# Performance work log

Hardware: AMD Instinct MI355X
Metric: run time of the kernel (lower is better)

Reference implementation:

```python
import jax, jax.numpy as jnp
import numpy as np

EPS = 1e-8

def _squash(t, axis=-1):
    sq = jnp.sum(t * t, axis=axis, keepdims=True)
    return (sq / (1.0 + sq)) * t / jnp.sqrt(sq + EPS)

def setup_inputs() -> dict:
    key = jax.random.key(0)
    k1, k2 = jax.random.split(key)
    B, IC, NC, OD, ID = 128, 2048, 16, 16, 8
    x = jax.random.normal(k1, (B, IC, ID), dtype=jnp.float32)
    W = 0.01 * jax.random.normal(k2, (1, IC, NC, OD, ID), dtype=jnp.float32)
    return {"x": x, "W": W}

def reference(x, W):
    # u_hat[b,i,c,o] = sum_d W[0,i,c,o,d] * x[b,i,d]
    u_hat = jnp.einsum('icod,bid->bico', W[0], x)  # [B, IC, NC, OD]
    B, IC, NC, _ = u_hat.shape
    b_ij = jnp.zeros((B, IC, NC, 1), dtype=u_hat.dtype)
    v_j = None
    for _ in range(3):  # fixed 3 routing iterations
        c_ij = jax.nn.softmax(b_ij, axis=2)                 # [B, IC, NC, 1]
        s_j = jnp.sum(c_ij * u_hat, axis=1, keepdims=True)  # [B, 1, NC, OD]
        v_j = _squash(s_j, axis=-1)                          # [B, 1, NC, OD]
        b_ij = b_ij + jnp.sum(u_hat * v_j, axis=-1, keepdims=True)
    return jnp.squeeze(v_j, axis=1)  # [B, NC, OD]
```

## Files before the change

### kernel.cpp

```cpp
#include <hip/hip_runtime.h>
#include <math.h>

#define IC_   2048
#define NC_   16
#define OD_   16
#define ID_   8
#define B_    128
#define LOG2E_ 1.4426950408889634f

#define P1_BB   8
#define P1_CH   64
#define P1_ICPB (IC_/P1_CH)
#define P2_NCH  16

typedef _Float16 h2 __attribute__((ext_vector_type(2)));
typedef _Float16 h8 __attribute__((ext_vector_type(8)));

__device__ __forceinline__ int origco(int lane, int k) {
  return ((lane & 15) << 4) + (lane >> 4) + 4 * k;
}

template<int CTRL>
__device__ __forceinline__ float dpp_add(float x) {
  const int xi = __builtin_bit_cast(int, x);
  const int yi = __builtin_amdgcn_update_dpp(xi, xi, CTRL, 0xF, 0xF, false);
  return x + __builtin_bit_cast(float, yi);
}
__device__ __forceinline__ float row16_sum(float x) {
  x = dpp_add<0x0B1>(x);
  x = dpp_add<0x04E>(x);
  x = dpp_add<0x141>(x);
  x = dpp_add<0x140>(x);
  return x;
}

__device__ __forceinline__ float dot8h(h8 w, h8 x) {
  const h2 w0 = __builtin_shufflevector(w, w, 0, 1), x0 = __builtin_shufflevector(x, x, 0, 1);
  const h2 w1 = __builtin_shufflevector(w, w, 2, 3), x1 = __builtin_shufflevector(x, x, 2, 3);
  const h2 w2 = __builtin_shufflevector(w, w, 4, 5), x2 = __builtin_shufflevector(x, x, 4, 5);
  const h2 w3 = __builtin_shufflevector(w, w, 6, 7), x3 = __builtin_shufflevector(x, x, 6, 7);
  float s = __builtin_amdgcn_fdot2(w0, x0, 0.f, false);
  s = __builtin_amdgcn_fdot2(w1, x1, s, false);
  s = __builtin_amdgcn_fdot2(w2, x2, s, false);
  s = __builtin_amdgcn_fdot2(w3, x3, s, false);
  return s;
}

__device__ __forceinline__ unsigned int packh2(float a, float b) {
  h2 h; h[0] = (_Float16)a; h[1] = (_Float16)b;
  return __builtin_bit_cast(unsigned int, h);
}

__global__ __launch_bounds__(256)
void cvtWX(const float* __restrict__ W, const float* __restrict__ x,
           _Float16* __restrict__ Wh, _Float16* __restrict__ xh) {
  if (blockIdx.x < 2048) {
    const int idx = blockIdx.x * 256 + threadIdx.x;
    const int ro  = idx & 255;
    const int i   = idx >> 8;
    const int rp  = (ro >> 4) + ((ro & 3) << 4) + (((ro >> 2) & 3) << 6);
    const float4 a = ((const float4*)W)[2 * idx];
    const float4 b = ((const float4*)W)[2 * idx + 1];
    h8 h;
    h[0] = (_Float16)a.x; h[1] = (_Float16)a.y; h[2] = (_Float16)a.z; h[3] = (_Float16)a.w;
    h[4] = (_Float16)b.x; h[5] = (_Float16)b.y; h[6] = (_Float16)b.z; h[7] = (_Float16)b.w;
    *(h8*)(Wh + ((size_t)i * 256 + rp) * ID_) = h;
  } else {
    const int idx = (blockIdx.x - 2048) * 256 + threadIdx.x;
    const float4 a = ((const float4*)x)[2 * idx];
    const float4 b = ((const float4*)x)[2 * idx + 1];
    h8 h;
    h[0] = (_Float16)a.x; h[1] = (_Float16)a.y; h[2] = (_Float16)a.z; h[3] = (_Float16)a.w;
    h[4] = (_Float16)b.x; h[5] = (_Float16)b.y; h[6] = (_Float16)b.z; h[7] = (_Float16)b.w;
    ((h8*)xh)[idx] = h;
  }
}

__global__ __launch_bounds__(256)
void caps_pass1(const _Float16* __restrict__ xh, const _Float16* __restrict__ Wp,
                unsigned int* __restrict__ u_hat, float* __restrict__ s_part) {
  const int bg = blockIdx.x;
  const int ch = blockIdx.y;
  const int tid = threadIdx.x, wid = tid >> 6, lane = tid & 63;

  float acc[P1_BB][4];
#pragma unroll
  for (int bb = 0; bb < P1_BB; ++bb)
#pragma unroll
    for (int k = 0; k < 4; ++k) acc[bb][k] = 0.f;

  for (int t = 0; t < 4; ++t) {
    const int ip = ch * P1_ICPB + t * 8 + wid * 2;
    const _Float16* wr0 = Wp + (size_t)ip * 2048 + lane * ID_;
    const _Float16* wr1 = wr0 + 2048;
    const h8 wA0 = *(const h8*)(wr0);
    const h8 wA1 = *(const h8*)(wr0 + 512);
    const h8 wA2 = *(const h8*)(wr0 + 1024);
    const h8 wA3 = *(const h8*)(wr0 + 1536);
    const h8 wB0 = *(const h8*)(wr1);
    const h8 wB1 = *(const h8*)(wr1 + 512);
    const h8 wB2 = *(const h8*)(wr1 + 1024);
    const h8 wB3 = *(const h8*)(wr1 + 1536);

#pragma unroll
    for (int bb = 0; bb < P1_BB; ++bb) {
      const int b = bg * P1_BB + bb;
      const _Float16* xp = xh + ((size_t)b * IC_ + ip) * ID_;
      const h8 xv0 = *(const h8*)(xp);
      const h8 xv1 = *(const h8*)(xp + ID_);

      const float u00 = dot8h(wA0, xv0);
      const float u01 = dot8h(wA1, xv0);
      const float u02 = dot8h(wA2, xv0);
      const float u03 = dot8h(wA3, xv0);
      const float u10 = dot8h(wB0, xv1);
      const float u11 = dot8h(wB1, xv1);
      const float u12 = dot8h(wB2, xv1);
      const float u13 = dot8h(wB3, xv1);

      acc[bb][0] += u00 + u10;
      acc[bb][1] += u01 + u11;
      acc[bb][2] += u02 + u12;
      acc[bb][3] += u03 + u13;

      uint4 q;
      q.x = packh2(u00, u01);
      q.y = packh2(u02, u03);
      q.z = packh2(u10, u11);
      q.w = packh2(u12, u13);
      *(uint4*)(u_hat + ((size_t)b * 1024 + (ip >> 1)) * 256 + lane * 4) = q;
    }
  }

  __shared__ float red[4][P1_BB][272];
#pragma unroll
  for (int bb = 0; bb < P1_BB; ++bb)
#pragma unroll
    for (int k = 0; k < 4; ++k)
      red[wid][bb][((lane >> 4) + 4 * k) * 17 + (lane & 15)] = acc[bb][k];
  __syncthreads();
#pragma unroll
  for (int bb = 0; bb < P1_BB; ++bb) {
    const int addr = (tid & 15) * 17 + (tid >> 4);
    const float s = red[0][bb][addr] + red[1][bb][addr] + red[2][bb][addr] + red[3][bb][addr];
    s_part[((size_t)(bg * P1_BB + bb) * P1_CH + ch) * 256 + tid] = s;
  }
}

__global__ __launch_bounds__(256)
void caps_wpass(const unsigned int* __restrict__ u_hat, const float* __restrict__ vs,
                float* __restrict__ s_part) {
  const int b   = blockIdx.x;
  const int ich = blockIdx.y;
  const int tid = threadIdx.x, wid = tid >> 6, lane = tid & 63;

  const float vv0 = vs[b * 256 + origco(lane, 0)];
  const float vv1 = vs[b * 256 + origco(lane, 1)];
  const float vv2 = vs[b * 256 + origco(lane, 2)];
  const float vv3 = vs[b * 256 + origco(lane, 3)];

  float a0 = 0.f, a1 = 0.f, a2 = 0.f, a3 = 0.f;
  const unsigned int* up =
      u_hat + ((size_t)b * 1024 + ich * 64 + wid * 16) * 256 + lane * 4;

#pragma unroll 4
  for (int t = 0; t < 16; ++t) {
    const uint4 q = *(const uint4*)(up + (size_t)t * 256);

    {
      const h2 ha = __builtin_bit_cast(h2, q.x);
      const h2 hb = __builtin_bit_cast(h2, q.y);
      const float u0 = (float)ha[0], u1 = (float)ha[1];
      const float u2 = (float)hb[0], u3 = (float)hb[1];
      float p = u0 * vv0;
      p = fmaf(u1, vv1, p);
      p = fmaf(u2, vv2, p);
      p = fmaf(u3, vv3, p);
      p += __shfl_xor(p, 16);
      p += __shfl_xor(p, 32);
      const float e = __builtin_amdgcn_exp2f(p);
      const float Z = row16_sum(e);
      const float w = e * __builtin_amdgcn_rcpf(Z);
      a0 = fmaf(w, u0, a0);
      a1 = fmaf(w, u1, a1);
      a2 = fmaf(w, u2, a2);
      a3 = fmaf(w, u3, a3);
    }
    {
      const h2 ha = __builtin_bit_cast(h2, q.z);
      const h2 hb = __builtin_bit_cast(h2, q.w);
      const float u0 = (float)ha[0], u1 = (float)ha[1];
      const float u2 = (float)hb[0], u3 = (float)hb[1];
      float p = u0 * vv0;
      p = fmaf(u1, vv1, p);
      p = fmaf(u2, vv2, p);
      p = fmaf(u3, vv3, p);
      p += __shfl_xor(p, 16);
      p += __shfl_xor(p, 32);
      const float e = __builtin_amdgcn_exp2f(p);
      const float Z = row16_sum(e);
      const float w = e * __builtin_amdgcn_rcpf(Z);
      a0 = fmaf(w, u0, a0);
      a1 = fmaf(w, u1, a1);
      a2 = fmaf(w, u2, a2);
      a3 = fmaf(w, u3, a3);
    }
  }

  __shared__ float red[4][272];
  red[wid][((lane >> 4) + 0) * 17 + (lane & 15)]  = a0;
  red[wid][((lane >> 4) + 4) * 17 + (lane & 15)]  = a1;
  red[wid][((lane >> 4) + 8) * 17 + (lane & 15)]  = a2;
  red[wid][((lane >> 4) + 12) * 17 + (lane & 15)] = a3;
  __syncthreads();
  const int addr = (tid & 15) * 17 + (tid >> 4);
  const float s = red[0][addr] + red[1][addr] + red[2][addr] + red[3][addr];
  s_part[((size_t)b * P2_NCH + ich) * 256 + tid] = s;
}

__global__ __launch_bounds__(256)
void caps_reduce(const float* __restrict__ s_part, float* __restrict__ vraw,
                 float* __restrict__ vs_next, float* __restrict__ out,
                 const float* __restrict__ v_prev_raw, float scale, int mode, int nch) {
  const int b = blockIdx.x, t = threadIdx.x;
  float s = 0.f;
  for (int ch = 0; ch < nch; ++ch)
    s += s_part[((size_t)b * nch + ch) * 256 + t];
  s *= scale;
  float sq = s * s;
  sq += __shfl_xor(sq, 1); sq += __shfl_xor(sq, 2);
  sq += __shfl_xor(sq, 4); sq += __shfl_xor(sq, 8);
  const float f = sq / ((1.f + sq) * sqrtf(sq + 1e-8f));
  const float v = s * f;
  if (mode == 0) { vraw[b*256+t] = v; vs_next[b*256+t] = v * LOG2E_; }
  else if (mode == 1) { vs_next[b*256+t] = (v + v_prev_raw[b*256+t]) * LOG2E_; }
  else { out[b*256+t] = v; }
}

__device__ __forceinline__ float4 ld4(const float* p) { return *(const float4*)p; }
__device__ __forceinline__ float dot8f(float4 a0, float4 a1, float4 b0, float4 b1) {
  float s = a0.x * b0.x;
  s = fmaf(a0.y, b0.y, s); s = fmaf(a0.z, b0.z, s); s = fmaf(a0.w, b0.w, s);
  s = fmaf(a1.x, b1.x, s); s = fmaf(a1.y, b1.y, s); s = fmaf(a1.z, b1.z, s);
  s = fmaf(a1.w, b1.w, s);
  return s;
}
template<bool UNIFORM, int CH>
__global__ __launch_bounds__(256)
void caps_pass_f32(const float* __restrict__ x, const float* __restrict__ W,
                   const float* __restrict__ vs, float* __restrict__ s_part) {
  constexpr int ICPB  = IC_ / CH;
  constexpr int TITER = ICPB / 4;
  const int bg = blockIdx.x, ch = blockIdx.y, tid = threadIdx.x;
  const int wid = tid >> 6, lane = tid & 63;
  float4 vr[4];
  if (!UNIFORM) {
#pragma unroll
    for (int bb = 0; bb < 4; ++bb) {
      const float* vp = vs + (size_t)(bg * 4 + bb) * 256 + lane;
      vr[bb] = make_float4(vp[0], vp[64], vp[128], vp[192]);
    }
  }
  float4 acc[4];
#pragma unroll
  for (int bb = 0; bb < 4; ++bb) acc[bb] = make_float4(0.f, 0.f, 0.f, 0.f);
  for (int t = 0; t < TITER; ++t) {
    const int i = ch * ICPB + t * 4 + wid;
    const float* wr = W + (size_t)i * 2048 + lane * 8;
    const float4 wa0 = ld4(wr);        const float4 wa1 = ld4(wr + 4);
    const float4 wb0 = ld4(wr + 512);  const float4 wb1 = ld4(wr + 516);
    const float4 wc0 = ld4(wr + 1024); const float4 wc1 = ld4(wr + 1028);
    const float4 wd0 = ld4(wr + 1536); const float4 wd1 = ld4(wr + 1540);
#pragma unroll
    for (int bb = 0; bb < 4; ++bb) {
      const float* xp = x + ((size_t)(bg * 4 + bb) * IC_ + i) * ID_;
      const float4 x0 = ld4(xp), x1 = ld4(xp + 4);
      const float u0 = dot8f(wa0, wa1, x0, x1);
      const float u1 = dot8f(wb0, wb1, x0, x1);
      const float u2 = dot8f(wc0, wc1, x0, x1);
      const float u3 = dot8f(wd0, wd1, x0, x1);
      if (UNIFORM) {
        acc[bb].x += u0; acc[bb].y += u1; acc[bb].z += u2; acc[bb].w += u3;
      } else {
        const float d0 = row16_sum(u0 * vr[bb].x);
        const float d1 = row16_sum(u1 * vr[bb].y);
        const float d2 = row16_sum(u2 * vr[bb].z);
        const float d3 = row16_sum(u3 * vr[bb].w);
        const float e0 = __builtin_amdgcn_exp2f(d0);
        const float e1 = __builtin_amdgcn_exp2f(d1);
        const float e2 = __builtin_amdgcn_exp2f(d2);
        const float e3 = __builtin_amdgcn_exp2f(d3);
        float Z = (e0 + e1) + (e2 + e3);
        Z += __shfl_xor(Z, 16); Z += __shfl_xor(Z, 32);
        const float rr = __builtin_amdgcn_rcpf(Z);
        acc[bb].x = fmaf(e0 * rr, u0, acc[bb].x);
        acc[bb].y = fmaf(e1 * rr, u1, acc[bb].y);
        acc[bb].z = fmaf(e2 * rr, u2, acc[bb].z);
        acc[bb].w = fmaf(e3 * rr, u3, acc[bb].w);
      }
    }
  }
  __shared__ float red[4][4 * 256];
#pragma unroll
  for (int bb = 0; bb < 4; ++bb) {
    red[wid][bb * 256 + lane]       = acc[bb].x;
    red[wid][bb * 256 + lane + 64]  = acc[bb].y;
    red[wid][bb * 256 + lane + 128] = acc[bb].z;
    red[wid][bb * 256 + lane + 192] = acc[bb].w;
  }
  __syncthreads();
#pragma unroll
  for (int bb = 0; bb < 4; ++bb) {
    const int idx = bb * 256 + tid;
    const float s = red[0][idx] + red[1][idx] + red[2][idx] + red[3][idx];
    s_part[((size_t)(bg * 4 + bb) * CH + ch) * 256 + tid] = s;
  }
}

extern "C" void kernel_launch(void* const* d_in, const int* in_sizes, int n_in,
                              void* d_out, int out_size, void* d_ws, size_t ws_size,
                              hipStream_t stream) {
  (void)in_sizes; (void)n_in; (void)out_size;

  const float* x = (const float*)d_in[0];
  const float* W = (const float*)d_in[1];
  float* out = (float*)d_out;

  const size_t u_dw  = (size_t)B_ * 1024 * 256;
  const size_t sp_f  = (size_t)B_ * P1_CH * 256;
  const size_t v_f   = (size_t)B_ * 256;
  const size_t nW    = (size_t)IC_ * 256 * ID_;
  const size_t nX    = (size_t)B_ * IC_ * ID_;
  const size_t need  = u_dw * 4 + sp_f * 4 + 2 * v_f * 4 + (nW + nX) * 2;

  const dim3 blk(256), gridR(B_);

  if (ws_size >= need) {
    unsigned int* u_hat = (unsigned int*)d_ws;
    float* s_part = (float*)(u_hat + u_dw);
    float* v1raw  = s_part + sp_f;
    float* vsb    = v1raw + v_f;
    _Float16* Wh  = (_Float16*)(vsb + v_f);
    _Float16* xh  = Wh + nW;

    cvtWX<<<3072, blk, 0, stream>>>(W, x, Wh, xh);

    caps_pass1<<<dim3(B_ / P1_BB, P1_CH), blk, 0, stream>>>(xh, Wh, u_hat, s_part);
    caps_reduce<<<gridR, blk, 0, stream>>>(s_part, v1raw, vsb, nullptr, nullptr,
                                           1.f / 16.f, 0, P1_CH);
    caps_wpass<<<dim3(B_, P2_NCH), blk, 0, stream>>>(u_hat, vsb, s_part);
    caps_reduce<<<gridR, blk, 0, stream>>>(s_part, nullptr, vsb, nullptr, v1raw,
                                           1.f, 1, P2_NCH);
    caps_wpass<<<dim3(B_, P2_NCH), blk, 0, stream>>>(u_hat, vsb, s_part);
    caps_reduce<<<gridR, blk, 0, stream>>>(s_part, nullptr, nullptr, out, nullptr,
                                           1.f, 2, P2_NCH);
  } else {
    constexpr int CH = 32;
    float* s_part = (float*)d_ws;
    float* v1raw  = s_part + (size_t)B_ * CH * 256;
    float* vsb    = v1raw + (size_t)B_ * 256;
    const dim3 gridP(B_ / 4, CH);
    caps_pass_f32<true , CH><<<gridP, blk, 0, stream>>>(x, W, nullptr, s_part);
    caps_reduce<<<gridR, blk, 0, stream>>>(s_part, v1raw, vsb, nullptr, nullptr, 1.f/16.f, 0, CH);
    caps_pass_f32<false, CH><<<gridP, blk, 0, stream>>>(x, W, vsb, s_part);
    caps_reduce<<<gridR, blk, 0, stream>>>(s_part, nullptr, vsb, nullptr, v1raw, 1.f, 1, CH);
    caps_pass_f32<false, CH><<<gridP, blk, 0, stream>>>(x, W, vsb, s_part);
    caps_reduce<<<gridR, blk, 0, stream>>>(s_part, nullptr, nullptr, out, nullptr, 1.f, 2, CH);
  }
}
```

Baseline: 126.0 us.

## Process batch in two chunks to shrink the u_hat working set

Splits the routing pipeline into two batch chunks of 64, so the fp16 u_hat buffer and partial sums only hold half the batch at a time. The aim is to keep u_hat resident in the large last-level cache between pass1 and the two weighting passes, rather than streaming it from HBM. The weighting pass now uses 32 IC chunks of 8 rows per wave with a fully unrolled loop, which keeps its grid size per chunk the same as before. The cost is twice as many kernel launches and half-size grids for pass1 and the reduce kernels, which may leave parts of the GPU idle.

```diff
diff --git a/kernel.cpp b/kernel.cpp
--- a/kernel.cpp
+++ b/kernel.cpp
@@ -6,12 +6,14 @@
 #define OD_   16
 #define ID_   8
 #define B_    128
+#define CB_   64
 #define LOG2E_ 1.4426950408889634f
 
 #define P1_BB   8
+#define P1_BG   (CB_/P1_BB)
 #define P1_CH   64
 #define P1_ICPB (IC_/P1_CH)
-#define P2_NCH  16
+#define P2_NCH  32
 
 typedef _Float16 h2 __attribute__((ext_vector_type(2)));
 typedef _Float16 h8 __attribute__((ext_vector_type(8)));
@@ -78,7 +80,7 @@
 
 __global__ __launch_bounds__(256)
 void caps_pass1(const _Float16* __restrict__ xh, const _Float16* __restrict__ Wp,
-                unsigned int* __restrict__ u_hat, float* __restrict__ s_part) {
+                unsigned int* __restrict__ u_hat, float* __restrict__ s_part, int b0) {
   const int bg = blockIdx.x;
   const int ch = blockIdx.y;
   const int tid = threadIdx.x, wid = tid >> 6, lane = tid & 63;
@@ -104,7 +106,8 @@
 
 #pragma unroll
     for (int bb = 0; bb < P1_BB; ++bb) {
-      const int b = bg * P1_BB + bb;
+      const int bl = bg * P1_BB + bb;
+      const int b  = b0 + bl;
       const _Float16* xp = xh + ((size_t)b * IC_ + ip) * ID_;
       const h8 xv0 = *(const h8*)(xp);
       const h8 xv1 = *(const h8*)(xp + ID_);
@@ -128,7 +131,7 @@
       q.y = packh2(u02, u03);
       q.z = packh2(u10, u11);
       q.w = packh2(u12, u13);
-      *(uint4*)(u_hat + ((size_t)b * 1024 + (ip >> 1)) * 256 + lane * 4) = q;
+      *(uint4*)(u_hat + ((size_t)bl * 1024 + (ip >> 1)) * 256 + lane * 4) = q;
     }
   }
 
@@ -149,8 +152,9 @@
 
 __global__ __launch_bounds__(256)
 void caps_wpass(const unsigned int* __restrict__ u_hat, const float* __restrict__ vs,
-                float* __restrict__ s_part) {
-  const int b   = blockIdx.x;
+                float* __restrict__ s_part, int b0) {
+  const int bl  = blockIdx.x;
+  const int b   = b0 + bl;
   const int ich = blockIdx.y;
   const int tid = threadIdx.x, wid = tid >> 6, lane = tid & 63;
 
@@ -161,10 +165,10 @@
 
   float a0 = 0.f, a1 = 0.f, a2 = 0.f, a3 = 0.f;
   const unsigned int* up =
-      u_hat + ((size_t)b * 1024 + ich * 64 + wid * 16) * 256 + lane * 4;
-
-#pragma unroll 4
-  for (int t = 0; t < 16; ++t) {
+      u_hat + ((size_t)bl * 1024 + ich * 32 + wid * 8) * 256 + lane * 4;
+
+#pragma unroll
+  for (int t = 0; t < 8; ++t) {
     const uint4 q = *(const uint4*)(up + (size_t)t * 256);
 
     {
@@ -215,17 +219,19 @@
   __syncthreads();
   const int addr = (tid & 15) * 17 + (tid >> 4);
   const float s = red[0][addr] + red[1][addr] + red[2][addr] + red[3][addr];
-  s_part[((size_t)b * P2_NCH + ich) * 256 + tid] = s;
+  s_part[((size_t)bl * P2_NCH + ich) * 256 + tid] = s;
 }
 
 __global__ __launch_bounds__(256)
 void caps_reduce(const float* __restrict__ s_part, float* __restrict__ vraw,
                  float* __restrict__ vs_next, float* __restrict__ out,
-                 const float* __restrict__ v_prev_raw, float scale, int mode, int nch) {
-  const int b = blockIdx.x, t = threadIdx.x;
+                 const float* __restrict__ v_prev_raw, float scale, int mode,
+                 int nch, int b0) {
+  const int bl = blockIdx.x, t = threadIdx.x;
+  const int b  = b0 + bl;
   float s = 0.f;
   for (int ch = 0; ch < nch; ++ch)
-    s += s_part[((size_t)b * nch + ch) * 256 + t];
+    s += s_part[((size_t)bl * nch + ch) * 256 + t];
   s *= scale;
   float sq = s * s;
   sq += __shfl_xor(sq, 1); sq += __shfl_xor(sq, 2);
@@ -326,14 +332,14 @@
   const float* W = (const float*)d_in[1];
   float* out = (float*)d_out;
 
-  const size_t u_dw  = (size_t)B_ * 1024 * 256;
-  const size_t sp_f  = (size_t)B_ * P1_CH * 256;
+  const size_t u_dw  = (size_t)CB_ * 1024 * 256;
+  const size_t sp_f  = (size_t)CB_ * P1_CH * 256;
   const size_t v_f   = (size_t)B_ * 256;
   const size_t nW    = (size_t)IC_ * 256 * ID_;
   const size_t nX    = (size_t)B_ * IC_ * ID_;
   const size_t need  = u_dw * 4 + sp_f * 4 + 2 * v_f * 4 + (nW + nX) * 2;
 
-  const dim3 blk(256), gridR(B_);
+  const dim3 blk(256);
 
   if (ws_size >= need) {
     unsigned int* u_hat = (unsigned int*)d_ws;
@@ -345,26 +351,29 @@
 
     cvtWX<<<3072, blk, 0, stream>>>(W, x, Wh, xh);
 
-    caps_pass1<<<dim3(B_ / P1_BB, P1_CH), blk, 0, stream>>>(xh, Wh, u_hat, s_part);
-    caps_reduce<<<gridR, blk, 0, stream>>>(s_part, v1raw, vsb, nullptr, nullptr,
-                                           1.f / 16.f, 0, P1_CH);
-    caps_wpass<<<dim3(B_, P2_NCH), blk, 0, stream>>>(u_hat, vsb, s_part);
-    caps_reduce<<<gridR, blk, 0, stream>>>(s_part, nullptr, vsb, nullptr, v1raw,
-                                           1.f, 1, P2_NCH);
-    caps_wpass<<<dim3(B_, P2_NCH), blk, 0, stream>>>(u_hat, vsb, s_part);
-    caps_reduce<<<gridR, blk, 0, stream>>>(s_part, nullptr, nullptr, out, nullptr,
-                                           1.f, 2, P2_NCH);
+    for (int c = 0; c < B_ / CB_; ++c) {
+      const int b0 = c * CB_;
+      caps_pass1<<<dim3(P1_BG, P1_CH), blk, 0, stream>>>(xh, Wh, u_hat, s_part, b0);
+      caps_reduce<<<CB_, blk, 0, stream>>>(s_part, v1raw, vsb, nullptr, nullptr,
+                                           1.f / 16.f, 0, P1_CH, b0);
+      caps_wpass<<<dim3(CB_, P2_NCH), blk, 0, stream>>>(u_hat, vsb, s_part, b0);
+      caps_reduce<<<CB_, blk, 0, stream>>>(s_part, nullptr, vsb, nullptr, v1raw,
+                                           1.f, 1, P2_NCH, b0);
+      caps_wpass<<<dim3(CB_, P2_NCH), blk, 0, stream>>>(u_hat, vsb, s_part, b0);
+      caps_reduce<<<CB_, blk, 0, stream>>>(s_part, nullptr, nullptr, out, nullptr,
+                                           1.f, 2, P2_NCH, b0);
+    }
   } else {
     constexpr int CH = 32;
     float* s_part = (float*)d_ws;
     float* v1raw  = s_part + (size_t)B_ * CH * 256;
     float* vsb    = v1raw + (size_t)B_ * 256;
-    const dim3 gridP(B_ / 4, CH);
+    const dim3 gridP(B_ / 4, CH), gridR(B_);
     caps_pass_f32<true , CH><<<gridP, blk, 0, stream>>>(x, W, nullptr, s_part);
-    caps_reduce<<<gridR, blk, 0, stream>>>(s_part, v1raw, vsb, nullptr, nullptr, 1.f/16.f, 0, CH);
+    caps_reduce<<<gridR, blk, 0, stream>>>(s_part, v1raw, vsb, nullptr, nullptr, 1.f/16.f, 0, CH, 0);
     caps_pass_f32<false, CH><<<gridP, blk, 0, stream>>>(x, W, vsb, s_part);
-    caps_reduce<<<gridR, blk, 0, stream>>>(s_part, nullptr, vsb, nullptr, v1raw, 1.f, 1, CH);
+    caps_reduce<<<gridR, blk, 0, stream>>>(s_part, nullptr, vsb, nullptr, v1raw, 1.f, 1, CH, 0);
     caps_pass_f32<false, CH><<<gridP, blk, 0, stream>>>(x, W, vsb, s_part);
-    caps_reduce<<<gridR, blk, 0, stream>>>(s_part, nullptr, nullptr, out, nullptr, 1.f, 2, CH);
-  }
-}
+    caps_reduce<<<gridR, blk, 0, stream>>>(s_part, nullptr, nullptr, out, nullptr, 1.f, 2, CH, 0);
+  }
+}
```

After: 173.7 us. 37.9% more time.

## Defer u_hat materialization to second routing pass and fuse with weighted sum

Applied to the files above, without the earlier changes.

The first pass now only computes the uniform-weight sums without writing u_hat. The second routing iteration recomputes u_hat from the fp16 W and x, writes it out, and applies the softmax-weighted accumulation in the same kernel. This removes one full write-then-read round trip of the u_hat buffer at the cost of recomputing the dot products once more and adding register pressure from the per-batch v values.

```diff
diff --git a/kernel.cpp b/kernel.cpp
--- a/kernel.cpp
+++ b/kernel.cpp
@@ -49,6 +49,19 @@
 __device__ __forceinline__ unsigned int packh2(float a, float b) {
   h2 h; h[0] = (_Float16)a; h[1] = (_Float16)b;
   return __builtin_bit_cast(unsigned int, h);
+}
+
+__device__ __forceinline__ float smax_w(float u0, float u1, float u2, float u3,
+                                        const float* vv) {
+  float p = u0 * vv[0];
+  p = fmaf(u1, vv[1], p);
+  p = fmaf(u2, vv[2], p);
+  p = fmaf(u3, vv[3], p);
+  p += __shfl_xor(p, 16);
+  p += __shfl_xor(p, 32);
+  const float e = __builtin_amdgcn_exp2f(p);
+  const float Z = row16_sum(e);
+  return e * __builtin_amdgcn_rcpf(Z);
 }
 
 __global__ __launch_bounds__(256)
@@ -77,8 +90,8 @@
 }
 
 __global__ __launch_bounds__(256)
-void caps_pass1(const _Float16* __restrict__ xh, const _Float16* __restrict__ Wp,
-                unsigned int* __restrict__ u_hat, float* __restrict__ s_part) {
+void caps_sum1(const _Float16* __restrict__ xh, const _Float16* __restrict__ Wp,
+               float* __restrict__ s_part) {
   const int bg = blockIdx.x;
   const int ch = blockIdx.y;
   const int tid = threadIdx.x, wid = tid >> 6, lane = tid & 63;
@@ -108,6 +121,68 @@
       const _Float16* xp = xh + ((size_t)b * IC_ + ip) * ID_;
       const h8 xv0 = *(const h8*)(xp);
       const h8 xv1 = *(const h8*)(xp + ID_);
+      acc[bb][0] += dot8h(wA0, xv0) + dot8h(wB0, xv1);
+      acc[bb][1] += dot8h(wA1, xv0) + dot8h(wB1, xv1);
+      acc[bb][2] += dot8h(wA2, xv0) + dot8h(wB2, xv1);
+      acc[bb][3] += dot8h(wA3, xv0) + dot8h(wB3, xv1);
+    }
+  }
+
+  __shared__ float red[4][P1_BB][272];
+#pragma unroll
+  for (int bb = 0; bb < P1_BB; ++bb)
+#pragma unroll
+    for (int k = 0; k < 4; ++k)
+      red[wid][bb][((lane >> 4) + 4 * k) * 17 + (lane & 15)] = acc[bb][k];
+  __syncthreads();
+#pragma unroll
+  for (int bb = 0; bb < P1_BB; ++bb) {
+    const int addr = (tid & 15) * 17 + (tid >> 4);
+    const float s = red[0][bb][addr] + red[1][bb][addr] + red[2][bb][addr] + red[3][bb][addr];
+    s_part[((size_t)(bg * P1_BB + bb) * P1_CH + ch) * 256 + tid] = s;
+  }
+}
+
+__global__ __launch_bounds__(256)
+void caps_pass1w(const _Float16* __restrict__ xh, const _Float16* __restrict__ Wp,
+                 const float* __restrict__ vs, unsigned int* __restrict__ u_hat,
+                 float* __restrict__ s_part) {
+  const int bg = blockIdx.x;
+  const int ch = blockIdx.y;
+  const int tid = threadIdx.x, wid = tid >> 6, lane = tid & 63;
+
+  float vv[P1_BB][4];
+#pragma unroll
+  for (int bb = 0; bb < P1_BB; ++bb)
+#pragma unroll
+    for (int k = 0; k < 4; ++k)
+      vv[bb][k] = vs[(bg * P1_BB + bb) * 256 + origco(lane, k)];
+
+  float acc[P1_BB][4];
+#pragma unroll
+  for (int bb = 0; bb < P1_BB; ++bb)
+#pragma unroll
+    for (int k = 0; k < 4; ++k) acc[bb][k] = 0.f;
+
+  for (int t = 0; t < 4; ++t) {
+    const int ip = ch * P1_ICPB + t * 8 + wid * 2;
+    const _Float16* wr0 = Wp + (size_t)ip * 2048 + lane * ID_;
+    const _Float16* wr1 = wr0 + 2048;
+    const h8 wA0 = *(const h8*)(wr0);
+    const h8 wA1 = *(const h8*)(wr0 + 512);
+    const h8 wA2 = *(const h8*)(wr0 + 1024);
+    const h8 wA3 = *(const h8*)(wr0 + 1536);
+    const h8 wB0 = *(const h8*)(wr1);
+    const h8 wB1 = *(const h8*)(wr1 + 512);
+    const h8 wB2 = *(const h8*)(wr1 + 1024);
+    const h8 wB3 = *(const h8*)(wr1 + 1536);
+
+#pragma unroll
+    for (int bb = 0; bb < P1_BB; ++bb) {
+      const int b = bg * P1_BB + bb;
+      const _Float16* xp = xh + ((size_t)b * IC_ + ip) * ID_;
+      const h8 xv0 = *(const h8*)(xp);
+      const h8 xv1 = *(const h8*)(xp + ID_);
 
       const float u00 = dot8h(wA0, xv0);
       const float u01 = dot8h(wA1, xv0);
@@ -118,17 +193,23 @@
       const float u12 = dot8h(wB2, xv1);
       const float u13 = dot8h(wB3, xv1);
 
-      acc[bb][0] += u00 + u10;
-      acc[bb][1] += u01 + u11;
-      acc[bb][2] += u02 + u12;
-      acc[bb][3] += u03 + u13;
-
       uint4 q;
       q.x = packh2(u00, u01);
       q.y = packh2(u02, u03);
       q.z = packh2(u10, u11);
       q.w = packh2(u12, u13);
       *(uint4*)(u_hat + ((size_t)b * 1024 + (ip >> 1)) * 256 + lane * 4) = q;
+
+      const float w0 = smax_w(u00, u01, u02, u03, vv[bb]);
+      acc[bb][0] = fmaf(w0, u00, acc[bb][0]);
+      acc[bb][1] = fmaf(w0, u01, acc[bb][1]);
+      acc[bb][2] = fmaf(w0, u02, acc[bb][2]);
+      acc[bb][3] = fmaf(w0, u03, acc[bb][3]);
+      const float w1 = smax_w(u10, u11, u12, u13, vv[bb]);
+      acc[bb][0] = fmaf(w1, u10, acc[bb][0]);
+      acc[bb][1] = fmaf(w1, u11, acc[bb][1]);
+      acc[bb][2] = fmaf(w1, u12, acc[bb][2]);
+      acc[bb][3] = fmaf(w1, u13, acc[bb][3]);
     }
   }
 
@@ -154,10 +235,9 @@
   const int ich = blockIdx.y;
   const int tid = threadIdx.x, wid = tid >> 6, lane = tid & 63;
 
-  const float vv0 = vs[b * 256 + origco(lane, 0)];
-  const float vv1 = vs[b * 256 + origco(lane, 1)];
-  const float vv2 = vs[b * 256 + origco(lane, 2)];
-  const float vv3 = vs[b * 256 + origco(lane, 3)];
+  float vv[4];
+#pragma unroll
+  for (int k = 0; k < 4; ++k) vv[k] = vs[b * 256 + origco(lane, k)];
 
   float a0 = 0.f, a1 = 0.f, a2 = 0.f, a3 = 0.f;
   const unsigned int* up =
@@ -166,21 +246,12 @@
 #pragma unroll 4
   for (int t = 0; t < 16; ++t) {
     const uint4 q = *(const uint4*)(up + (size_t)t * 256);
-
     {
       const h2 ha = __builtin_bit_cast(h2, q.x);
       const h2 hb = __builtin_bit_cast(h2, q.y);
       const float u0 = (float)ha[0], u1 = (float)ha[1];
       const float u2 = (float)hb[0], u3 = (float)hb[1];
-      float p = u0 * vv0;
-      p = fmaf(u1, vv1, p);
-      p = fmaf(u2, vv2, p);
-      p = fmaf(u3, vv3, p);
-      p += __shfl_xor(p, 16);
-      p += __shfl_xor(p, 32);
-      const float e = __builtin_amdgcn_exp2f(p);
-      const float Z = row16_sum(e);
-      const float w = e * __builtin_amdgcn_rcpf(Z);
+      const float w = smax_w(u0, u1, u2, u3, vv);
       a0 = fmaf(w, u0, a0);
       a1 = fmaf(w, u1, a1);
       a2 = fmaf(w, u2, a2);
@@ -191,15 +262,7 @@
       const h2 hb = __builtin_bit_cast(h2, q.w);
       const float u0 = (float)ha[0], u1 = (float)ha[1];
       const float u2 = (float)hb[0], u3 = (float)hb[1];
-      float p = u0 * vv0;
-      p = fmaf(u1, vv1, p);
-      p = fmaf(u2, vv2, p);
-      p = fmaf(u3, vv3, p);
-      p += __shfl_xor(p, 16);
-      p += __shfl_xor(p, 32);
-      const float e = __builtin_amdgcn_exp2f(p);
-      const float Z = row16_sum(e);
-      const float w = e * __builtin_amdgcn_rcpf(Z);
+      const float w = smax_w(u0, u1, u2, u3, vv);
       a0 = fmaf(w, u0, a0);
       a1 = fmaf(w, u1, a1);
       a2 = fmaf(w, u2, a2);
@@ -345,12 +408,12 @@
 
     cvtWX<<<3072, blk, 0, stream>>>(W, x, Wh, xh);
 
-    caps_pass1<<<dim3(B_ / P1_BB, P1_CH), blk, 0, stream>>>(xh, Wh, u_hat, s_part);
+    caps_sum1<<<dim3(B_ / P1_BB, P1_CH), blk, 0, stream>>>(xh, Wh, s_part);
     caps_reduce<<<gridR, blk, 0, stream>>>(s_part, v1raw, vsb, nullptr, nullptr,
                                            1.f / 16.f, 0, P1_CH);
-    caps_wpass<<<dim3(B_, P2_NCH), blk, 0, stream>>>(u_hat, vsb, s_part);
+    caps_pass1w<<<dim3(B_ / P1_BB, P1_CH), blk, 0, stream>>>(xh, Wh, vsb, u_hat, s_part);
     caps_reduce<<<gridR, blk, 0, stream>>>(s_part, nullptr, vsb, nullptr, v1raw,
-                                           1.f, 1, P2_NCH);
+                                           1.f, 1, P1_CH);
     caps_wpass<<<dim3(B_, P2_NCH), blk, 0, stream>>>(u_hat, vsb, s_part);
     caps_reduce<<<gridR, blk, 0, stream>>>(s_part, nullptr, nullptr, out, nullptr,
                                            1.f, 2, P2_NCH);
```

Result: slower. 149.5 us (+18.7%).
